# Kernel optimization log

Measured on AMD Instinct MI355X. Metric: run time of the kernel, lower is better.

Reference implementation:

```python
import jax, jax.numpy as jnp
import numpy as np

# ---- model constants (match init_kwargs) ----
E = 128; GH = 8; GD = E // GH; GL = 3          # graph emb / heads / layers
SH = 4; SD = E // SH; SL = 4                   # sequence transformer
ATOM = 64; BOND = 16; RBF_K = 32; CUTOFF = 5.0
VOCAB = 64; SEQL = 128
N = 32                                          # nodes per graph (equal-size graphs)
GC = 64; GS = 16; BMOL = 16; DEG = 64; GF = 3   # conf graphs / scaffold graphs / molecules / edges-per-graph
LN_EPS = 1e-5
CENTERS = jnp.linspace(0.0, CUTOFF, RBF_K)
GAMMA = (CUTOFF / (RBF_K - 1)) ** -2            # GaussianRBF gamma = (center spacing)^-2


def _ln(x, g, b):
    mu = x.mean(-1, keepdims=True)
    var = ((x - mu) ** 2).mean(-1, keepdims=True)
    return (x - mu) / jnp.sqrt(var + LN_EPS) * g + b


def _graph_encoder(x, edge_index, edge_attr, pos, G, p):
    # node projection
    h = x @ p["gproj_w"] + p["gproj_b"]                      # [G*N, E]
    # edge features: bond features + RBF(distance)
    d = jnp.clip(edge_attr[:, -1], 0.0, 10.0)
    rbf = jnp.exp(-GAMMA * (d[:, None] - CENTERS) ** 2)       # [M, K]
    ef = jnp.concatenate([edge_attr[:, :-1], rbf], axis=1)    # [M, BOND+K]
    # EdgeNetwork: per-edge matrix (gather -> matvec -> scatter-add)
    M = ef.shape[0]
    m = (ef @ p["elin_w"] + p["elin_b"]).reshape(M, E, E)
    msg = jnp.einsum("mef,mf->me", m, h[edge_index[1]])      # [M, E]
    aggr = jnp.zeros_like(h).at[edge_index[0]].add(msg)
    h = _ln(h + aggr, p["eln_g"], p["eln_b"])
    # dense per-graph layout (equal-size graphs -> reshape, mask is all-true)
    hb = h.reshape(G, N, E)
    pp = pos.reshape(G, N, 3)
    d2 = jnp.sum((pp[:, :, None, :] - pp[:, None, :, :]) ** 2, axis=-1)
    dist = jnp.where(d2 > 0, jnp.sqrt(jnp.where(d2 > 0, d2, 1.0)), 0.0)  # safe cdist
    inv_sqrt_d = 1.0 / np.sqrt(GD)
    for l in range(GL):
        def heads(t):
            return t.reshape(G, N, GH, GD).transpose(0, 2, 1, 3)
        q = heads(hb @ p["gt_qw"][l] + p["gt_qb"][l])
        k = heads(hb @ p["gt_kw"][l] + p["gt_kb"][l])
        v = heads(hb @ p["gt_vw"][l] + p["gt_vb"][l])
        s = jnp.einsum("bhnd,bhmd->bhnm", q, k) * inv_sqrt_d + dist[:, None]
        s = jnp.clip(s, -10.0, 10.0)
        a = jax.nn.softmax(s, axis=-1)                       # all nodes valid -> no mask
        o = jnp.einsum("bhnm,bhmd->bhnd", a, v).transpose(0, 2, 1, 3).reshape(G, N, E)
        o = o @ p["gt_ow"][l] + p["gt_ob"][l]
        x1 = _ln(hb + o, p["gt_ln1g"][l], p["gt_ln1b"][l])
        ff = jax.nn.relu(x1 @ p["gt_f1w"][l] + p["gt_f1b"][l]) @ p["gt_f2w"][l] + p["gt_f2b"][l]
        hb = _ln(x1 + ff, p["gt_ln2g"][l], p["gt_ln2b"][l])
    # masked mean pool with the source's eps in the denominator
    return hb.sum(1) / (N + 1e-8)


def _seq_encoder(tokens, p):
    B, L = tokens.shape
    x = p["tok_emb"][tokens] + p["pos_emb"][:L][None]        # [B, L, E]
    inv_sqrt_d = 1.0 / np.sqrt(SD)
    for l in range(SL):
        qkv = x @ p["se_inw"][l] + p["se_inb"][l]            # [B, L, 3E]
        q, k, v = jnp.split(qkv, 3, axis=-1)
        def heads(t):
            return t.reshape(B, L, SH, SD).transpose(0, 2, 1, 3)
        q, k, v = heads(q), heads(k), heads(v)
        a = jax.nn.softmax(jnp.einsum("bhnd,bhmd->bhnm", q, k) * inv_sqrt_d, axis=-1)
        o = jnp.einsum("bhnm,bhmd->bhnd", a, v).transpose(0, 2, 1, 3).reshape(B, L, E)
        o = o @ p["se_ow"][l] + p["se_ob"][l]
        x = _ln(x + o, p["se_ln1g"][l], p["se_ln1b"][l])      # post-norm (torch default)
        ff = jax.nn.relu(x @ p["se_f1w"][l] + p["se_f1b"][l]) @ p["se_f2w"][l] + p["se_f2b"][l]
        x = _ln(x + ff, p["se_ln2g"][l], p["se_ln2b"][l])
    return x.mean(1)                                          # [B, E]


def _forward(p, conf_edge_index, scaf_edge_index, tokens, conf_per_mol):
    g_all = _graph_encoder(p["conf_x"], conf_edge_index, p["conf_edge_attr"], p["conf_pos"], GC, p)
    conf_emb = g_all.reshape(-1, conf_per_mol, E).mean(1)     # per-molecule conformer mean (equal counts)
    scaf_emb = _graph_encoder(p["scaf_x"], scaf_edge_index, p["scaf_edge_attr"], p["scaf_pos"], GS, p)
    total = conf_emb + scaf_emb
    seq = _seq_encoder(tokens, p)
    # FusionGating
    gate_h = jax.nn.relu(jnp.concatenate([total, seq], -1) @ p["fg1_w"] + p["fg1_b"])
    gate = jax.nn.sigmoid(gate_h @ p["fg2_w"] + p["fg2_b"])
    fused = gate * total + (1.0 - gate) * seq
    # CrossModalAttention: MHA over a length-1 sequence (unsqueeze(0)) -> softmax
    # weights are identically 1, so attn(q_in, kv, kv) == out_proj(v_proj(kv)).
    g, s = fused, fused
    for l in range(2):
        g2s = (s @ p["cm_g2s_vw"][l] + p["cm_g2s_vb"][l]) @ p["cm_g2s_ow"][l] + p["cm_g2s_ob"][l]
        g = _ln(g + g2s, p["cm_n1g"][l], p["cm_n1b"][l])
        s2g = (g @ p["cm_s2g_vw"][l] + p["cm_s2g_vb"][l]) @ p["cm_s2g_ow"][l] + p["cm_s2g_ob"][l]
        s = _ln(s + s2g, p["cm_n2g"][l], p["cm_n2b"][l])
    final = (g + s) * 0.5
    comb = jnp.concatenate([final, p["graph_features"]], -1)
    return (jax.nn.relu(comb @ p["r1_w"] + p["r1_b"]) @ p["r2_w"] + p["r2_b"])[:, 0]


def setup_inputs() -> dict:
    ks = iter(jax.random.split(jax.random.key(0), 64))
    def nrm(shape, s):
        return (jax.random.normal(next(ks), shape) * s).astype(jnp.float32)
    inp = {}
    def mk_graph(prefix, G):
        inp[prefix + "_x"] = nrm((G * N, ATOM), 1.0)
        off = (jnp.arange(G) * N)[:, None]
        src = jax.random.randint(next(ks), (G, DEG), 0, N) + off   # within-graph edges
        dst = jax.random.randint(next(ks), (G, DEG), 0, N) + off
        inp[prefix + "_edge_index"] = jnp.stack([src.ravel(), dst.ravel()]).astype(jnp.int32)
        bond = jax.random.uniform(next(ks), (G * DEG, BOND))
        dist = jax.random.uniform(next(ks), (G * DEG, 1), minval=0.5, maxval=CUTOFF)
        inp[prefix + "_edge_attr"] = jnp.concatenate([bond, dist], 1).astype(jnp.float32)
        inp[prefix + "_pos"] = nrm((G * N, 3), 2.0)
    mk_graph("conf", GC)
    mk_graph("scaf", GS)
    inp["tokens"] = jax.random.randint(next(ks), (BMOL, SEQL), 1, VOCAB).astype(jnp.int32)
    inp["graph_features"] = nrm((BMOL, GF), 1.0)
    inp["conf_per_mol"] = GC // BMOL
    W = 0.05
    inp["gproj_w"] = nrm((ATOM, E), W); inp["gproj_b"] = jnp.zeros(E)
    inp["elin_w"] = nrm((BOND + RBF_K, E * E), W); inp["elin_b"] = jnp.zeros(E * E)
    inp["eln_g"] = jnp.ones(E); inp["eln_b"] = jnp.zeros(E)
    for nm in ["qw", "kw", "vw", "ow"]:
        inp["gt_" + nm] = nrm((GL, E, E), W)
        inp["gt_" + nm[0] + "b"] = jnp.zeros((GL, E))
    inp["gt_ln1g"] = jnp.ones((GL, E)); inp["gt_ln1b"] = jnp.zeros((GL, E))
    inp["gt_f1w"] = nrm((GL, E, 2 * E), W); inp["gt_f1b"] = jnp.zeros((GL, 2 * E))
    inp["gt_f2w"] = nrm((GL, 2 * E, E), W); inp["gt_f2b"] = jnp.zeros((GL, E))
    inp["gt_ln2g"] = jnp.ones((GL, E)); inp["gt_ln2b"] = jnp.zeros((GL, E))
    inp["tok_emb"] = nrm((VOCAB, E), 0.02); inp["pos_emb"] = nrm((256, E), 0.02)
    inp["se_inw"] = nrm((SL, E, 3 * E), W); inp["se_inb"] = jnp.zeros((SL, 3 * E))
    inp["se_ow"] = nrm((SL, E, E), W); inp["se_ob"] = jnp.zeros((SL, E))
    inp["se_ln1g"] = jnp.ones((SL, E)); inp["se_ln1b"] = jnp.zeros((SL, E))
    inp["se_f1w"] = nrm((SL, E, 2 * E), W); inp["se_f1b"] = jnp.zeros((SL, 2 * E))
    inp["se_f2w"] = nrm((SL, 2 * E, E), W); inp["se_f2b"] = jnp.zeros((SL, E))
    inp["se_ln2g"] = jnp.ones((SL, E)); inp["se_ln2b"] = jnp.zeros((SL, E))
    inp["fg1_w"] = nrm((2 * E, 64), W); inp["fg1_b"] = jnp.zeros(64)
    inp["fg2_w"] = nrm((64, E), W); inp["fg2_b"] = jnp.zeros(E)
    for nm in ["g2s", "s2g"]:
        inp["cm_" + nm + "_vw"] = nrm((2, E, E), W); inp["cm_" + nm + "_vb"] = jnp.zeros((2, E))
        inp["cm_" + nm + "_ow"] = nrm((2, E, E), W); inp["cm_" + nm + "_ob"] = jnp.zeros((2, E))
    inp["cm_n1g"] = jnp.ones((2, E)); inp["cm_n1b"] = jnp.zeros((2, E))
    inp["cm_n2g"] = jnp.ones((2, E)); inp["cm_n2b"] = jnp.zeros((2, E))
    inp["r1_w"] = nrm((E + GF, E), W); inp["r1_b"] = jnp.zeros(E)
    inp["r2_w"] = nrm((E, 1), W); inp["r2_b"] = jnp.zeros(1)
    return inp


def reference(conf_x, conf_edge_attr, conf_pos, scaf_x, scaf_edge_attr, scaf_pos, graph_features,
              gproj_w, gproj_b, elin_w, elin_b, eln_g, eln_b,
              gt_qw, gt_qb, gt_kw, gt_kb, gt_vw, gt_vb, gt_ow, gt_ob,
              gt_ln1g, gt_ln1b, gt_f1w, gt_f1b, gt_f2w, gt_f2b, gt_ln2g, gt_ln2b,
              tok_emb, pos_emb,
              se_inw, se_inb, se_ow, se_ob, se_ln1g, se_ln1b, se_f1w, se_f1b, se_f2w, se_f2b, se_ln2g, se_ln2b,
              fg1_w, fg1_b, fg2_w, fg2_b,
              cm_g2s_vw, cm_g2s_vb, cm_g2s_ow, cm_g2s_ob, cm_n1g, cm_n1b,
              cm_s2g_vw, cm_s2g_vb, cm_s2g_ow, cm_s2g_ob, cm_n2g, cm_n2b,
              r1_w, r1_b, r2_w, r2_b,
              conf_edge_index, scaf_edge_index, tokens, conf_per_mol):
    p = dict(locals())
    return _forward(p, conf_edge_index, scaf_edge_index, tokens, conf_per_mol)
```

## Files before the change

### kernel.cpp

```cpp
#include <hip/hip_runtime.h>
#include <hip/hip_bf16.h>


struct __align__(16) G16Sm   { float Sa[32][20]; float Bs[32][136]; };
struct __align__(16) GAttnSm { float qs[32][17], ksh[32][17], vsh[32][17], ss[32][33], rs[32]; };
struct __align__(16) SAttnSm { float kv[32][33], qs2[32][33], ss2[32][129], red[32][8], red2[32][8]; };
struct __align__(16) TailSm  { float x1[16][132]; float hid[16][260]; float sbuf[4352]; float Sa[32][20]; };
union AttnU { GAttnSm a; SAttnSm s; };

__device__ __forceinline__ float blk_norm(float v, int e, float* sred)
{
  float s = v;
  #pragma unroll
  for (int o = 1; o < 64; o <<= 1) s += __shfl_xor(s, o);
  if ((e & 63) == 0) sred[e >> 6] = s;
  __syncthreads();
  float mean = (sred[0] + sred[1]) * (1.0f / 128.0f);
  __syncthreads();
  float d = v - mean;
  float s2 = d * d;
  #pragma unroll
  for (int o = 1; o < 64; o <<= 1) s2 += __shfl_xor(s2, o);
  if ((e & 63) == 0) sred[e >> 6] = s2;
  __syncthreads();
  float var = (sred[0] + sred[1]) * (1.0f / 128.0f);
  __syncthreads();
  return d / sqrtf(var + 1e-5f);
}

__global__ __launch_bounds__(256) void front_k(
    const float* __restrict__ cx, const float* __restrict__ sx,
    const float* __restrict__ w, const float* __restrict__ b,
    float* __restrict__ h, float* __restrict__ aggr,
    const float* __restrict__ cpos, const float* __restrict__ spos, float* __restrict__ dist,
    const int* __restrict__ tokens, const float* __restrict__ tok_emb,
    const float* __restrict__ pos_emb, float* __restrict__ xs)
{
  __shared__ float sP[128];
  const int bx = blockIdx.x, tid = threadIdx.x;
  if (bx < 1280) {
    int r = bx * 2 + (tid >> 7), e = tid & 127;
    const float* x = (r < 2048) ? (cx + (size_t)r * 64) : (sx + (size_t)(r - 2048) * 64);
    float* xrow = sP + (tid >> 7) * 64;
    if (e < 64) xrow[e] = x[e];
    __syncthreads();
    float acc = b[e];
    for (int a = 0; a < 64; a++) acc += xrow[a] * w[a * 128 + e];
    h[(size_t)r * 128 + e] = acc;
    aggr[(size_t)r * 128 + e] = 0.0f;
  } else if (bx < 1360) {
    int g = bx - 1280;
    const float* p = (g < 64) ? (cpos + (size_t)g * 96) : (spos + (size_t)(g - 64) * 96);
    if (tid < 96) sP[tid] = p[tid];
    __syncthreads();
    #pragma unroll
    for (int jj = 0; jj < 4; jj++) {
      int idx = tid * 4 + jj;
      int i = idx >> 5, j = idx & 31;
      float dx = sP[i * 3 + 0] - sP[j * 3 + 0];
      float dy = sP[i * 3 + 1] - sP[j * 3 + 1];
      float dz = sP[i * 3 + 2] - sP[j * 3 + 2];
      float d2 = dx * dx + dy * dy + dz * dz;
      dist[(size_t)g * 1024 + idx] = (d2 > 0.0f) ? sqrtf(d2) : 0.0f;
    }
  } else {
    int r = (bx - 1360) * 2 + (tid >> 7), e = tid & 127;
    int tk = tokens[r];
    xs[(size_t)r * 128 + e] = tok_emb[(size_t)tk * 128 + e] + pos_emb[(size_t)(r & 127) * 128 + e];
  }
}

__global__ __launch_bounds__(256) void edge_gemm_k(
    const float* __restrict__ cea, const float* __restrict__ sea,
    const int* __restrict__ cei, const int* __restrict__ sei,
    const float* __restrict__ h,
    const float* __restrict__ elw, const float* __restrict__ elb,
    float* __restrict__ aggr)
{
  __shared__ float efs[32][8];
  __shared__ float As[32][36];
  __shared__ float Bs[32][136];
  const int tid = threadIdx.x;
  const int m0 = blockIdx.x * 32;
  const int kt0 = blockIdx.y * 28;
  const int c0 = kt0 >> 2;
  {
    int t = tid >> 3, cc = tid & 7;
    if (cc < 7) {
      int c = c0 + cc;
      int m = m0 + t;
      const float* attr = (m < 4096) ? (cea + (size_t)m * 17) : (sea + (size_t)(m - 4096) * 17);
      float val;
      if (c < 16) val = attr[c];
      else if (c < 48) {
        float d = fminf(fmaxf(attr[16], 0.0f), 10.0f);
        float t2 = d - (float)((c - 16) * (5.0 / 31.0));
        val = expf(-38.44f * t2 * t2);
      } else val = 1.0f;
      efs[t][cc] = val;
    }
  }
  const int gk = tid & 31, gt = (tid >> 5) * 4;
  float hreg[4][4];
  #pragma unroll
  for (int i = 0; i < 4; i++) {
    int m = m0 + gt + i;
    int dst = (m < 4096) ? cei[4096 + m] : (sei[1024 + (m - 4096)] + 2048);
    const float* hp = h + (size_t)dst * 128 + gk;
    hreg[i][0] = hp[0]; hreg[i][1] = hp[32]; hreg[i][2] = hp[64]; hreg[i][3] = hp[96];
  }
  const int tn = tid & 31, tm = tid >> 5;
  const int e0 = 4 * tn, t0 = 4 * tm;
  const int se = tid >> 1, sk = (tid & 1) * 16;
  float acc[4][4] = {};
  __syncthreads();
  #pragma unroll 1
  for (int kt = kt0; kt < kt0 + 28; kt++) {
    int c = kt >> 2, cc = c - c0, j = kt & 3;
    float4 av;
    av.x = efs[gt + 0][cc] * hreg[0][j];
    av.y = efs[gt + 1][cc] * hreg[1][j];
    av.z = efs[gt + 2][cc] * hreg[2][j];
    av.w = efs[gt + 3][cc] * hreg[3][j];
    *(float4*)&As[gk][gt] = av;
    const float* bp = ((c < 48) ? (elw + (size_t)c * 16384) : elb) + (size_t)se * 128 + j * 32 + sk;
    float4 w0 = *(const float4*)(bp + 0);
    float4 w1 = *(const float4*)(bp + 4);
    float4 w2 = *(const float4*)(bp + 8);
    float4 w3 = *(const float4*)(bp + 12);
    Bs[sk + 0][se] = w0.x;  Bs[sk + 1][se] = w0.y;  Bs[sk + 2][se] = w0.z;  Bs[sk + 3][se] = w0.w;
    Bs[sk + 4][se] = w1.x;  Bs[sk + 5][se] = w1.y;  Bs[sk + 6][se] = w1.z;  Bs[sk + 7][se] = w1.w;
    Bs[sk + 8][se] = w2.x;  Bs[sk + 9][se] = w2.y;  Bs[sk + 10][se] = w2.z; Bs[sk + 11][se] = w2.w;
    Bs[sk + 12][se] = w3.x; Bs[sk + 13][se] = w3.y; Bs[sk + 14][se] = w3.z; Bs[sk + 15][se] = w3.w;
    __syncthreads();
    #pragma unroll
    for (int kk = 0; kk < 32; kk++) {
      float4 a = *(const float4*)&As[kk][t0];
      float4 b = *(const float4*)&Bs[kk][e0];
      acc[0][0] += a.x * b.x; acc[0][1] += a.x * b.y; acc[0][2] += a.x * b.z; acc[0][3] += a.x * b.w;
      acc[1][0] += a.y * b.x; acc[1][1] += a.y * b.y; acc[1][2] += a.y * b.z; acc[1][3] += a.y * b.w;
      acc[2][0] += a.z * b.x; acc[2][1] += a.z * b.y; acc[2][2] += a.z * b.z; acc[2][3] += a.z * b.w;
      acc[3][0] += a.w * b.x; acc[3][1] += a.w * b.y; acc[3][2] += a.w * b.z; acc[3][3] += a.w * b.w;
    }
    __syncthreads();
  }
  #pragma unroll
  for (int i = 0; i < 4; i++) {
    int m = m0 + t0 + i;
    int src = (m < 4096) ? cei[m] : (sei[m - 4096] + 2048);
    float* dst = aggr + (size_t)src * 128 + e0;
    atomicAdd(dst + 0, acc[i][0]);
    atomicAdd(dst + 1, acc[i][1]);
    atomicAdd(dst + 2, acc[i][2]);
    atomicAdd(dst + 3, acc[i][3]);
  }
}

__device__ __forceinline__ void gemm16_body(G16Sm& sm,
    const float* __restrict__ A, const float* __restrict__ Bp,
    const float* __restrict__ biasp, float* __restrict__ Cp,
    int row0, int ldb, int ldc)
{
  const int tid = threadIdx.x;
  const int tm = tid >> 5, tn = tid & 31;
  const int t0 = 2 * tm, e0 = 4 * tn;
  const int ar = tid >> 4, ak = (tid & 15) * 2;
  const int bk = tid >> 3, be = (tid & 7) * 16;
  float acc[2][4] = {};
  for (int k0 = 0; k0 < 128; k0 += 32) {
    float2 av = *(const float2*)(A + (size_t)(row0 + ar) * 128 + k0 + ak);
    sm.Sa[ak][ar] = av.x; sm.Sa[ak + 1][ar] = av.y;
    const float* bp = Bp + (size_t)(k0 + bk) * ldb + be;
    float4 b0v = *(const float4*)(bp + 0);
    float4 b1v = *(const float4*)(bp + 4);
    float4 b2v = *(const float4*)(bp + 8);
    float4 b3v = *(const float4*)(bp + 12);
    sm.Bs[bk][be + 0] = b0v.x;  sm.Bs[bk][be + 1] = b0v.y;  sm.Bs[bk][be + 2] = b0v.z;  sm.Bs[bk][be + 3] = b0v.w;
    sm.Bs[bk][be + 4] = b1v.x;  sm.Bs[bk][be + 5] = b1v.y;  sm.Bs[bk][be + 6] = b1v.z;  sm.Bs[bk][be + 7] = b1v.w;
    sm.Bs[bk][be + 8] = b2v.x;  sm.Bs[bk][be + 9] = b2v.y;  sm.Bs[bk][be + 10] = b2v.z; sm.Bs[bk][be + 11] = b2v.w;
    sm.Bs[bk][be + 12] = b3v.x; sm.Bs[bk][be + 13] = b3v.y; sm.Bs[bk][be + 14] = b3v.z; sm.Bs[bk][be + 15] = b3v.w;
    __syncthreads();
    #pragma unroll
    for (int kk = 0; kk < 32; kk++) {
      float2 a = *(const float2*)&sm.Sa[kk][t0];
      float4 b = *(const float4*)&sm.Bs[kk][e0];
      acc[0][0] += a.x * b.x; acc[0][1] += a.x * b.y; acc[0][2] += a.x * b.z; acc[0][3] += a.x * b.w;
      acc[1][0] += a.y * b.x; acc[1][1] += a.y * b.y; acc[1][2] += a.y * b.z; acc[1][3] += a.y * b.w;
    }
    __syncthreads();
  }
  #pragma unroll
  for (int i = 0; i < 2; i++) {
    float* cp = Cp + (size_t)(row0 + t0 + i) * ldc + e0;
    #pragma unroll
    for (int j = 0; j < 4; j++) cp[j] = acc[i][j] + biasp[e0 + j];
  }
}

__global__ __launch_bounds__(256) void qkv_k(
    int gBlocks,
    const float* __restrict__ ghb,
    const float* gqw, const float* gkw, const float* gvw,
    const float* gqb, const float* gkb, const float* gvb, float* gout,
    const float* __restrict__ sxs, const float* sw, const float* sb, float* sout)
{
  __shared__ G16Sm sm;
  int bx = blockIdx.x;
  if (bx < gBlocks) {
    int z = bx / 160, rt = bx % 160;
    const float* B = (z == 0) ? gqw : (z == 1) ? gkw : gvw;
    const float* bias = (z == 0) ? gqb : (z == 1) ? gkb : gvb;
    gemm16_body(sm, ghb, B, bias, gout + (size_t)z * 327680, rt * 16, 128, 128);
  } else {
    int i = bx - gBlocks;
    int z = i >> 7, rt = i & 127;
    gemm16_body(sm, sxs, sw + z * 128, sb + z * 128, sout + z * 128, rt * 16, 384, 384);
  }
}

__device__ __forceinline__ void gattn_body(GAttnSm& sm, int g, int h,
    const float* __restrict__ q, const float* __restrict__ k,
    const float* __restrict__ v, const float* __restrict__ dist, float* __restrict__ o)
{
  const int tid = threadIdx.x;
  {
    int idx = tid * 2;
    int i = idx >> 4, d = idx & 15;
    size_t base = ((size_t)(g * 32 + i)) * 128 + h * 16 + d;
    sm.qs[i][d] = q[base];  sm.qs[i][d + 1] = q[base + 1];
    sm.ksh[i][d] = k[base]; sm.ksh[i][d + 1] = k[base + 1];
    sm.vsh[i][d] = v[base]; sm.vsh[i][d + 1] = v[base + 1];
  }
  __syncthreads();
  {
    int i = tid >> 3, j0 = (tid & 7) * 4;
    for (int j = j0; j < j0 + 4; j++) {
      float a = 0;
      #pragma unroll
      for (int d = 0; d < 16; d++) a += sm.qs[i][d] * sm.ksh[j][d];
      a = a * 0.25f + dist[(size_t)g * 1024 + i * 32 + j];
      sm.ss[i][j] = fminf(fmaxf(a, -10.0f), 10.0f);
    }
  }
  __syncthreads();
  if (tid < 32) {
    float m = -1e30f;
    for (int j = 0; j < 32; j++) m = fmaxf(m, sm.ss[tid][j]);
    float s = 0;
    for (int j = 0; j < 32; j++) { float ex = expf(sm.ss[tid][j] - m); sm.ss[tid][j] = ex; s += ex; }
    sm.rs[tid] = 1.0f / s;
  }
  __syncthreads();
  {
    int idx = tid * 2;
    int i = idx >> 4, d = idx & 15;
    float a0 = 0, a1 = 0;
    for (int j = 0; j < 32; j++) { float wj = sm.ss[i][j]; a0 += wj * sm.vsh[j][d]; a1 += wj * sm.vsh[j][d + 1]; }
    float r = sm.rs[i];
    size_t base = ((size_t)(g * 32 + i)) * 128 + h * 16 + d;
    o[base] = a0 * r; o[base + 1] = a1 * r;
  }
}

__device__ __forceinline__ void sattn_body(SAttnSm& sm, int b, int h, int qt,
    const float* __restrict__ qkv, float* __restrict__ o)
{
  const int tid = threadIdx.x;
  {
    int i = tid >> 3, d0 = (tid & 7) * 4;
    const float* qp = qkv + ((size_t)(b * 128 + qt * 32 + i)) * 384 + h * 32 + d0;
    sm.qs2[i][d0 + 0] = qp[0]; sm.qs2[i][d0 + 1] = qp[1];
    sm.qs2[i][d0 + 2] = qp[2]; sm.qs2[i][d0 + 3] = qp[3];
  }
  const int i = tid >> 3, sub = tid & 7;
  for (int jt = 0; jt < 4; jt++) {
    {
      int r = tid >> 3, dd = (tid & 7) * 4;
      const float* kp = qkv + ((size_t)(b * 128 + jt * 32 + r)) * 384 + 128 + h * 32 + dd;
      float4 kv4 = *(const float4*)kp;
      sm.kv[r][dd + 0] = kv4.x; sm.kv[r][dd + 1] = kv4.y;
      sm.kv[r][dd + 2] = kv4.z; sm.kv[r][dd + 3] = kv4.w;
    }
    __syncthreads();
    {
      int j0 = jt * 32 + sub * 4;
      for (int j = j0; j < j0 + 4; j++) {
        int jr = j - jt * 32;
        float a = 0;
        #pragma unroll
        for (int d = 0; d < 32; d++) a += sm.qs2[i][d] * sm.kv[jr][d];
        sm.ss2[i][j] = a * 0.17677669529663687f;
      }
    }
    __syncthreads();
  }
  float m = -1e30f;
  for (int j = sub; j < 128; j += 8) m = fmaxf(m, sm.ss2[i][j]);
  sm.red[i][sub] = m;
  __syncthreads();
  float mm = sm.red[i][0];
  #pragma unroll
  for (int t = 1; t < 8; t++) mm = fmaxf(mm, sm.red[i][t]);
  float ps = 0;
  for (int j = sub; j < 128; j += 8) { float ex = expf(sm.ss2[i][j] - mm); sm.ss2[i][j] = ex; ps += ex; }
  sm.red2[i][sub] = ps;
  __syncthreads();
  float s = 0;
  #pragma unroll
  for (int t = 0; t < 8; t++) s += sm.red2[i][t];
  float rinv = 1.0f / s;
  float a0 = 0, a1 = 0, a2 = 0, a3 = 0;
  const int d0 = sub * 4;
  for (int jt = 0; jt < 4; jt++) {
    __syncthreads();
    {
      int r = tid >> 3, dd = (tid & 7) * 4;
      const float* vp = qkv + ((size_t)(b * 128 + jt * 32 + r)) * 384 + 256 + h * 32 + dd;
      float4 vv = *(const float4*)vp;
      sm.kv[r][dd + 0] = vv.x; sm.kv[r][dd + 1] = vv.y;
      sm.kv[r][dd + 2] = vv.z; sm.kv[r][dd + 3] = vv.w;
    }
    __syncthreads();
    for (int jr = 0; jr < 32; jr++) {
      float wj = sm.ss2[i][jt * 32 + jr];
      a0 += wj * sm.kv[jr][d0 + 0]; a1 += wj * sm.kv[jr][d0 + 1];
      a2 += wj * sm.kv[jr][d0 + 2]; a3 += wj * sm.kv[jr][d0 + 3];
    }
  }
  float* op = o + ((size_t)(b * 128 + qt * 32 + i)) * 128 + h * 32 + d0;
  op[0] = a0 * rinv; op[1] = a1 * rinv; op[2] = a2 * rinv; op[3] = a3 * rinv;
}

__global__ __launch_bounds__(256) void attn_k(
    int gBlocks, const float* q, const float* k, const float* v,
    const float* dist, float* go, const float* qkv, float* so)
{
  __shared__ AttnU u;
  int bx = blockIdx.x;
  if (bx < gBlocks) gattn_body(u.a, bx >> 3, bx & 7, q, k, v, dist, go);
  else { int i = bx - gBlocks; sattn_body(u.s, i >> 4, (i >> 2) & 3, i & 3, qkv, so); }
}

__device__ __forceinline__ void tail_body(TailSm& sm, int row0, const float* __restrict__ A,
    const float* __restrict__ Wo, const float* __restrict__ bo, const float* __restrict__ res,
    const float* __restrict__ g1, const float* __restrict__ b1n,
    const float* __restrict__ W1, const float* __restrict__ b1f,
    const float* __restrict__ W2, const float* __restrict__ b2f,
    const float* __restrict__ g2, const float* __restrict__ b2n,
    float* __restrict__ Out)
{
  float (*BsA)[136] = (float(*)[136])sm.sbuf;
  float (*Bs1)[260] = (float(*)[260])sm.sbuf;
  float (*Bs2)[136] = (float(*)[136])sm.sbuf;
  const int tid = threadIdx.x;
  {
    const int tm = tid >> 5, tn = tid & 31;
    const int t0 = 2 * tm, e0 = 4 * tn;
    const int ar = tid >> 4, ak = (tid & 15) * 2;
    const int bk = tid >> 3, be = (tid & 7) * 16;
    float acc[2][4] = {};
    for (int k0 = 0; k0 < 128; k0 += 32) {
      float2 av = *(const float2*)(A + (size_t)(row0 + ar) * 128 + k0 + ak);
      sm.Sa[ak][ar] = av.x; sm.Sa[ak + 1][ar] = av.y;
      const float* bp = Wo + (size_t)(k0 + bk) * 128 + be;
      float4 b0v = *(const float4*)(bp + 0);
      float4 b1v = *(const float4*)(bp + 4);
      float4 b2v = *(const float4*)(bp + 8);
      float4 b3v = *(const float4*)(bp + 12);
      BsA[bk][be + 0] = b0v.x;  BsA[bk][be + 1] = b0v.y;  BsA[bk][be + 2] = b0v.z;  BsA[bk][be + 3] = b0v.w;
      BsA[bk][be + 4] = b1v.x;  BsA[bk][be + 5] = b1v.y;  BsA[bk][be + 6] = b1v.z;  BsA[bk][be + 7] = b1v.w;
      BsA[bk][be + 8] = b2v.x;  BsA[bk][be + 9] = b2v.y;  BsA[bk][be + 10] = b2v.z; BsA[bk][be + 11] = b2v.w;
      BsA[bk][be + 12] = b3v.x; BsA[bk][be + 13] = b3v.y; BsA[bk][be + 14] = b3v.z; BsA[bk][be + 15] = b3v.w;
      __syncthreads();
      #pragma unroll
      for (int kk = 0; kk < 32; kk++) {
        float2 a = *(const float2*)&sm.Sa[kk][t0];
        float4 b = *(const float4*)&BsA[kk][e0];
        acc[0][0] += a.x * b.x; acc[0][1] += a.x * b.y; acc[0][2] += a.x * b.z; acc[0][3] += a.x * b.w;
        acc[1][0] += a.y * b.x; acc[1][1] += a.y * b.y; acc[1][2] += a.y * b.z; acc[1][3] += a.y * b.w;
      }
      __syncthreads();
    }
    #pragma unroll
    for (int i = 0; i < 2; i++) {
      int r = row0 + t0 + i;
      float v0 = acc[i][0] + bo[e0 + 0] + res[(size_t)r * 128 + e0 + 0];
      float v1 = acc[i][1] + bo[e0 + 1] + res[(size_t)r * 128 + e0 + 1];
      float v2 = acc[i][2] + bo[e0 + 2] + res[(size_t)r * 128 + e0 + 2];
      float v3 = acc[i][3] + bo[e0 + 3] + res[(size_t)r * 128 + e0 + 3];
      float s = v0 + v1 + v2 + v3;
      #pragma unroll
      for (int o = 1; o < 32; o <<= 1) s += __shfl_xor(s, o);
      float mean = s * (1.0f / 128.0f);
      float d0 = v0 - mean, d1 = v1 - mean, d2 = v2 - mean, d3 = v3 - mean;
      float sq = d0 * d0 + d1 * d1 + d2 * d2 + d3 * d3;
      #pragma unroll
      for (int o = 1; o < 32; o <<= 1) sq += __shfl_xor(sq, o);
      float rstd = 1.0f / sqrtf(sq * (1.0f / 128.0f) + 1e-5f);
      sm.x1[t0 + i][e0 + 0] = d0 * rstd * g1[e0 + 0] + b1n[e0 + 0];
      sm.x1[t0 + i][e0 + 1] = d1 * rstd * g1[e0 + 1] + b1n[e0 + 1];
      sm.x1[t0 + i][e0 + 2] = d2 * rstd * g1[e0 + 2] + b1n[e0 + 2];
      sm.x1[t0 + i][e0 + 3] = d3 * rstd * g1[e0 + 3] + b1n[e0 + 3];
    }
  }
  __syncthreads();
  {
    const int tm = tid >> 6, tn = tid & 63;
    const int t0 = 4 * tm, e0 = 4 * tn;
    const int ar = tid >> 4, ak = tid & 15;
    const int bk = tid >> 4, be = (tid & 15) * 16;
    float acc[4][4] = {};
    for (int k0 = 0; k0 < 128; k0 += 16) {
      sm.Sa[ak][ar] = sm.x1[ar][k0 + ak];
      const float* bp = W1 + (size_t)(k0 + bk) * 256 + be;
      float4 b0v = *(const float4*)(bp + 0);
      float4 b1v = *(const float4*)(bp + 4);
      float4 b2v = *(const float4*)(bp + 8);
      float4 b3v = *(const float4*)(bp + 12);
      Bs1[bk][be + 0] = b0v.x;  Bs1[bk][be + 1] = b0v.y;  Bs1[bk][be + 2] = b0v.z;  Bs1[bk][be + 3] = b0v.w;
      Bs1[bk][be + 4] = b1v.x;  Bs1[bk][be + 5] = b1v.y;  Bs1[bk][be + 6] = b1v.z;  Bs1[bk][be + 7] = b1v.w;
      Bs1[bk][be + 8] = b2v.x;  Bs1[bk][be + 9] = b2v.y;  Bs1[bk][be + 10] = b2v.z; Bs1[bk][be + 11] = b2v.w;
      Bs1[bk][be + 12] = b3v.x; Bs1[bk][be + 13] = b3v.y; Bs1[bk][be + 14] = b3v.z; Bs1[bk][be + 15] = b3v.w;
      __syncthreads();
      #pragma unroll
      for (int kk = 0; kk < 16; kk++) {
        float4 a = *(const float4*)&sm.Sa[kk][t0];
        float4 b = *(const float4*)&Bs1[kk][e0];
        acc[0][0] += a.x * b.x; acc[0][1] += a.x * b.y; acc[0][2] += a.x * b.z; acc[0][3] += a.x * b.w;
        acc[1][0] += a.y * b.x; acc[1][1] += a.y * b.y; acc[1][2] += a.y * b.z; acc[1][3] += a.y * b.w;
        acc[2][0] += a.z * b.x; acc[2][1] += a.z * b.y; acc[2][2] += a.z * b.z; acc[2][3] += a.z * b.w;
        acc[3][0] += a.w * b.x; acc[3][1] += a.w * b.y; acc[3][2] += a.w * b.z; acc[3][3] += a.w * b.w;
      }
      __syncthreads();
    }
    #pragma unroll
    for (int i = 0; i < 4; i++) {
      float4 hv;
      hv.x = fmaxf(acc[i][0] + b1f[e0 + 0], 0.0f);
      hv.y = fmaxf(acc[i][1] + b1f[e0 + 1], 0.0f);
      hv.z = fmaxf(acc[i][2] + b1f[e0 + 2], 0.0f);
      hv.w = fmaxf(acc[i][3] + b1f[e0 + 3], 0.0f);
      *(float4*)&sm.hid[t0 + i][e0] = hv;
    }
  }
  __syncthreads();
  {
    const int tm = tid >> 5, tn = tid & 31;
    const int t0 = 2 * tm, e0 = 4 * tn;
    const int bk = tid >> 3, be = (tid & 7) * 16;
    float acc[2][4] = {};
    for (int k0 = 0; k0 < 256; k0 += 32) {
      const float* bp = W2 + (size_t)(k0 + bk) * 128 + be;
      float4 b0v = *(const float4*)(bp + 0);
      float4 b1v = *(const float4*)(bp + 4);
      float4 b2v = *(const float4*)(bp + 8);
      float4 b3v = *(const float4*)(bp + 12);
      Bs2[bk][be + 0] = b0v.x;  Bs2[bk][be + 1] = b0v.y;  Bs2[bk][be + 2] = b0v.z;  Bs2[bk][be + 3] = b0v.w;
      Bs2[bk][be + 4] = b1v.x;  Bs2[bk][be + 5] = b1v.y;  Bs2[bk][be + 6] = b1v.z;  Bs2[bk][be + 7] = b1v.w;
      Bs2[bk][be + 8] = b2v.x;  Bs2[bk][be + 9] = b2v.y;  Bs2[bk][be + 10] = b2v.z; Bs2[bk][be + 11] = b2v.w;
      Bs2[bk][be + 12] = b3v.x; Bs2[bk][be + 13] = b3v.y; Bs2[bk][be + 14] = b3v.z; Bs2[bk][be + 15] = b3v.w;
      __syncthreads();
      #pragma unroll
      for (int kk = 0; kk < 32; kk++) {
        float a0 = sm.hid[t0 + 0][k0 + kk];
        float a1 = sm.hid[t0 + 1][k0 + kk];
        float4 b = *(const float4*)&Bs2[kk][e0];
        acc[0][0] += a0 * b.x; acc[0][1] += a0 * b.y; acc[0][2] += a0 * b.z; acc[0][3] += a0 * b.w;
        acc[1][0] += a1 * b.x; acc[1][1] += a1 * b.y; acc[1][2] += a1 * b.z; acc[1][3] += a1 * b.w;
      }
      __syncthreads();
    }
    #pragma unroll
    for (int i = 0; i < 2; i++) {
      int r = row0 + t0 + i;
      float v0 = acc[i][0] + b2f[e0 + 0] + sm.x1[t0 + i][e0 + 0];
      float v1 = acc[i][1] + b2f[e0 + 1] + sm.x1[t0 + i][e0 + 1];
      float v2 = acc[i][2] + b2f[e0 + 2] + sm.x1[t0 + i][e0 + 2];
      float v3 = acc[i][3] + b2f[e0 + 3] + sm.x1[t0 + i][e0 + 3];
      float s = v0 + v1 + v2 + v3;
      #pragma unroll
      for (int o = 1; o < 32; o <<= 1) s += __shfl_xor(s, o);
      float mean = s * (1.0f / 128.0f);
      float d0 = v0 - mean, d1 = v1 - mean, d2 = v2 - mean, d3 = v3 - mean;
      float sq = d0 * d0 + d1 * d1 + d2 * d2 + d3 * d3;
      #pragma unroll
      for (int o = 1; o < 32; o <<= 1) sq += __shfl_xor(sq, o);
      float rstd = 1.0f / sqrtf(sq * (1.0f / 128.0f) + 1e-5f);
      float* cp = Out + (size_t)r * 128 + e0;
      cp[0] = d0 * rstd * g2[e0 + 0] + b2n[e0 + 0];
      cp[1] = d1 * rstd * g2[e0 + 1] + b2n[e0 + 1];
      cp[2] = d2 * rstd * g2[e0 + 2] + b2n[e0 + 2];
      cp[3] = d3 * rstd * g2[e0 + 3] + b2n[e0 + 3];
    }
  }
}

__global__ __launch_bounds__(256) void tail_k(
    int gBlocks,
    const float* gA, const float* gWo, const float* gbo, const float* gres,
    const float* gg1, const float* gb1, const float* gW1, const float* gbf1,
    const float* gW2, const float* gbf2, const float* gg2, const float* gb2, float* gOut,
    const float* sA, const float* sWo, const float* sbo, const float* sres,
    const float* sg1, const float* sb1, const float* sW1, const float* sbf1,
    const float* sW2, const float* sbf2, const float* sg2, const float* sb2, float* sOut)
{
  __shared__ TailSm sm;
  int bx = blockIdx.x;
  if (bx < gBlocks)
    tail_body(sm, bx * 16, gA, gWo, gbo, gres, gg1, gb1, gW1, gbf1, gW2, gbf2, gg2, gb2, gOut);
  else
    tail_body(sm, (bx - gBlocks) * 16, sA, sWo, sbo, sres, sg1, sb1, sW1, sbf1, sW2, sbf2, sg2, sb2, sOut);
}

__global__ __launch_bounds__(128) void ln_k(
    const float* __restrict__ x, const float* __restrict__ res,
    const float* __restrict__ g, const float* __restrict__ b, float* __restrict__ out)
{
  __shared__ float sred[2];
  int r = blockIdx.x, e = threadIdx.x;
  size_t idx = (size_t)r * 128 + e;
  float v = x[idx] + res[idx];
  float nv = blk_norm(v, e, sred);
  out[idx] = nv * g[e] + b[e];
}

__global__ __launch_bounds__(128) void head_k(
    const float* __restrict__ hb, const float* __restrict__ xs, const float* __restrict__ gfeat,
    const float* fg1w, const float* fg1b, const float* fg2w, const float* fg2b,
    const float* g2s_vw, const float* g2s_vb, const float* g2s_ow, const float* g2s_ob,
    const float* n1g, const float* n1b,
    const float* s2g_vw, const float* s2g_vb, const float* s2g_ow, const float* s2g_ob,
    const float* n2g, const float* n2b,
    const float* r1w, const float* r1b, const float* r2w, const float* r2b,
    float* __restrict__ out)
{
  __shared__ float T[128], S[128], G[128], Sm[128], t1[128], t2[128], gh[64], sred[2];
  int mol = blockIdx.x, e = threadIdx.x;
  {
    float cs = 0;
    for (int c = 0; c < 4; c++) {
      int g = mol * 4 + c;
      float s = 0;
      for (int i = 0; i < 32; i++) s += hb[((size_t)(g * 32 + i)) * 128 + e];
      cs += s * (1.0f / 32.0f);
    }
    cs *= 0.25f;
    float s2 = 0;
    int g = 64 + mol;
    for (int i = 0; i < 32; i++) s2 += hb[((size_t)(g * 32 + i)) * 128 + e];
    T[e] = cs + s2 * (1.0f / 32.0f);
    float ss = 0;
    for (int l = 0; l < 128; l++) ss += xs[((size_t)(mol * 128 + l)) * 128 + e];
    S[e] = ss * (1.0f / 128.0f);
  }
  __syncthreads();
  if (e < 64) {
    float a = fg1b[e];
    for (int f = 0; f < 128; f++) a += T[f] * fg1w[f * 64 + e];
    for (int f = 0; f < 128; f++) a += S[f] * fg1w[(128 + f) * 64 + e];
    gh[e] = fmaxf(a, 0.0f);
  }
  __syncthreads();
  {
    float a = fg2b[e];
    for (int j = 0; j < 64; j++) a += gh[j] * fg2w[j * 128 + e];
    float gate = 1.0f / (1.0f + expf(-a));
    float fu = gate * T[e] + (1.0f - gate) * S[e];
    G[e] = fu; Sm[e] = fu;
  }
  __syncthreads();
  for (int l = 0; l < 2; l++) {
    const float* vw = g2s_vw + (size_t)l * 16384; const float* vb = g2s_vb + l * 128;
    const float* ow = g2s_ow + (size_t)l * 16384; const float* ob = g2s_ob + l * 128;
    float a = vb[e];
    for (int f = 0; f < 128; f++) a += Sm[f] * vw[f * 128 + e];
    t1[e] = a;
    __syncthreads();
    a = ob[e];
    for (int f = 0; f < 128; f++) a += t1[f] * ow[f * 128 + e];
    float nv = blk_norm(G[e] + a, e, sred);
    G[e] = nv * n1g[l * 128 + e] + n1b[l * 128 + e];
    __syncthreads();
    const float* vw2 = s2g_vw + (size_t)l * 16384; const float* vb2 = s2g_vb + l * 128;
    const float* ow2 = s2g_ow + (size_t)l * 16384; const float* ob2 = s2g_ob + l * 128;
    a = vb2[e];
    for (int f = 0; f < 128; f++) a += G[f] * vw2[f * 128 + e];
    t1[e] = a;
    __syncthreads();
    a = ob2[e];
    for (int f = 0; f < 128; f++) a += t1[f] * ow2[f * 128 + e];
    nv = blk_norm(Sm[e] + a, e, sred);
    Sm[e] = nv * n2g[l * 128 + e] + n2b[l * 128 + e];
    __syncthreads();
  }
  t2[e] = 0.5f * (G[e] + Sm[e]);
  __syncthreads();
  float a = r1b[e];
  for (int f = 0; f < 128; f++) a += t2[f] * r1w[f * 128 + e];
  for (int f = 0; f < 3; f++) a += gfeat[mol * 3 + f] * r1w[(128 + f) * 128 + e];
  a = fmaxf(a, 0.0f);
  float p = a * r2w[e];
  #pragma unroll
  for (int o = 1; o < 64; o <<= 1) p += __shfl_xor(p, o);
  if ((e & 63) == 0) sred[e >> 6] = p;
  __syncthreads();
  if (e == 0) out[mol] = sred[0] + sred[1] + r2b[0];
}

extern "C" void kernel_launch(void* const* d_in, const int* in_sizes, int n_in,
                              void* d_out, int out_size, void* d_ws, size_t ws_size,
                              hipStream_t stream)
{
  (void)n_in; (void)out_size; (void)ws_size;
  const bool dict = (in_sizes[1] == 8192);
  auto IN = [&](int di, int si) { return d_in[dict ? di : si]; };

  const float* conf_x   = (const float*)IN(0, 0);
  const int*   conf_ei  = (const int*)  IN(1, 63);
  const float* conf_ea  = (const float*)IN(2, 1);
  const float* conf_pos = (const float*)IN(3, 2);
  const float* scaf_x   = (const float*)IN(4, 3);
  const int*   scaf_ei  = (const int*)  IN(5, 64);
  const float* scaf_ea  = (const float*)IN(6, 4);
  const float* scaf_pos = (const float*)IN(7, 5);
  const int*   tokens   = (const int*)  IN(8, 65);
  const float* gfeat    = (const float*)IN(9, 6);
  const float* gproj_w  = (const float*)IN(11, 7);
  const float* gproj_b  = (const float*)IN(12, 8);
  const float* elin_w   = (const float*)IN(13, 9);
  const float* elin_b   = (const float*)IN(14, 10);
  const float* eln_g    = (const float*)IN(15, 11);
  const float* eln_b    = (const float*)IN(16, 12);
  const float* gt_qw    = (const float*)IN(17, 13);
  const float* gt_qb    = (const float*)IN(18, 14);
  const float* gt_kw    = (const float*)IN(19, 15);
  const float* gt_kb    = (const float*)IN(20, 16);
  const float* gt_vw    = (const float*)IN(21, 17);
  const float* gt_vb    = (const float*)IN(22, 18);
  const float* gt_ow    = (const float*)IN(23, 19);
  const float* gt_ob    = (const float*)IN(24, 20);
  const float* gt_ln1g  = (const float*)IN(25, 21);
  const float* gt_ln1b  = (const float*)IN(26, 22);
  const float* gt_f1w   = (const float*)IN(27, 23);
  const float* gt_f1b   = (const float*)IN(28, 24);
  const float* gt_f2w   = (const float*)IN(29, 25);
  const float* gt_f2b   = (const float*)IN(30, 26);
  const float* gt_ln2g  = (const float*)IN(31, 27);
  const float* gt_ln2b  = (const float*)IN(32, 28);
  const float* tok_emb  = (const float*)IN(33, 29);
  const float* pos_emb  = (const float*)IN(34, 30);
  const float* se_inw   = (const float*)IN(35, 31);
  const float* se_inb   = (const float*)IN(36, 32);
  const float* se_ow    = (const float*)IN(37, 33);
  const float* se_ob    = (const float*)IN(38, 34);
  const float* se_ln1g  = (const float*)IN(39, 35);
  const float* se_ln1b  = (const float*)IN(40, 36);
  const float* se_f1w   = (const float*)IN(41, 37);
  const float* se_f1b   = (const float*)IN(42, 38);
  const float* se_f2w   = (const float*)IN(43, 39);
  const float* se_f2b   = (const float*)IN(44, 40);
  const float* se_ln2g  = (const float*)IN(45, 41);
  const float* se_ln2b  = (const float*)IN(46, 42);
  const float* fg1_w    = (const float*)IN(47, 43);
  const float* fg1_b    = (const float*)IN(48, 44);
  const float* fg2_w    = (const float*)IN(49, 45);
  const float* fg2_b    = (const float*)IN(50, 46);
  const float* cm_g2s_vw = (const float*)IN(51, 47);
  const float* cm_g2s_vb = (const float*)IN(52, 48);
  const float* cm_g2s_ow = (const float*)IN(53, 49);
  const float* cm_g2s_ob = (const float*)IN(54, 50);
  const float* cm_s2g_vw = (const float*)IN(55, 53);
  const float* cm_s2g_vb = (const float*)IN(56, 54);
  const float* cm_s2g_ow = (const float*)IN(57, 55);
  const float* cm_s2g_ob = (const float*)IN(58, 56);
  const float* cm_n1g   = (const float*)IN(59, 51);
  const float* cm_n1b   = (const float*)IN(60, 52);
  const float* cm_n2g   = (const float*)IN(61, 57);
  const float* cm_n2b   = (const float*)IN(62, 58);
  const float* r1_w     = (const float*)IN(63, 59);
  const float* r1_b     = (const float*)IN(64, 60);
  const float* r2_w     = (const float*)IN(65, 61);
  const float* r2_b     = (const float*)IN(66, 62);
  float* out = (float*)d_out;

  float* w = (float*)d_ws;
  size_t off = 0;
  auto alloc = [&](size_t n) { float* p = w + off; off += n; return p; };
  float* h     = alloc(2560 * 128);
  float* aggr  = alloc(2560 * 128);
  float* hb    = alloc(2560 * 128);
  float* distb = alloc(80 * 1024);
  float* qb    = alloc(3 * 327680);
  float* atto  = alloc(327680);
  float* xs2   = alloc(2048 * 128);
  float* qkv3  = alloc(2048 * 384);
  float* satto = alloc(2048 * 128);
  float* xsfin = alloc(2048 * 128);

  front_k<<<2384, 256, 0, stream>>>(conf_x, scaf_x, gproj_w, gproj_b, h, aggr,
                                    conf_pos, scaf_pos, distb,
                                    tokens, tok_emb, pos_emb, xs2);
  edge_gemm_k<<<dim3(160, 7), 256, 0, stream>>>(conf_ea, scaf_ea, conf_ei, scaf_ei, h, elin_w, elin_b, aggr);
  ln_k<<<2560, 128, 0, stream>>>(aggr, h, eln_g, eln_b, hb);

  for (int l = 0; l < 4; l++) {
    const bool hasG = (l < 3);
    const int lg = hasG ? l : 0;
    const int gq = hasG ? 480 : 0;
    const int ga = hasG ? 640 : 0;
    const int gt = hasG ? 160 : 0;
    float* sOut = (l == 3) ? xsfin : xs2;
    qkv_k<<<gq + 384, 256, 0, stream>>>(gq,
        hb, gt_qw + (size_t)lg * 16384, gt_kw + (size_t)lg * 16384, gt_vw + (size_t)lg * 16384,
        gt_qb + lg * 128, gt_kb + lg * 128, gt_vb + lg * 128, qb,
        xs2, se_inw + (size_t)l * 49152, se_inb + l * 384, qkv3);
    attn_k<<<ga + 256, 256, 0, stream>>>(ga, qb, qb + 327680, qb + 655360, distb, atto, qkv3, satto);
    tail_k<<<gt + 128, 256, 0, stream>>>(gt,
        atto, gt_ow + (size_t)lg * 16384, gt_ob + lg * 128, hb,
        gt_ln1g + lg * 128, gt_ln1b + lg * 128,
        gt_f1w + (size_t)lg * 32768, gt_f1b + lg * 256,
        gt_f2w + (size_t)lg * 32768, gt_f2b + lg * 128,
        gt_ln2g + lg * 128, gt_ln2b + lg * 128, hb,
        satto, se_ow + (size_t)l * 16384, se_ob + l * 128, xs2,
        se_ln1g + l * 128, se_ln1b + l * 128,
        se_f1w + (size_t)l * 32768, se_f1b + l * 256,
        se_f2w + (size_t)l * 32768, se_f2b + l * 128,
        se_ln2g + l * 128, se_ln2b + l * 128, sOut);
  }

  head_k<<<16, 128, 0, stream>>>(hb, xsfin, gfeat,
                                 fg1_w, fg1_b, fg2_w, fg2_b,
                                 cm_g2s_vw, cm_g2s_vb, cm_g2s_ow, cm_g2s_ob, cm_n1g, cm_n1b,
                                 cm_s2g_vw, cm_s2g_vb, cm_s2g_ow, cm_s2g_ob, cm_n2g, cm_n2b,
                                 r1_w, r1_b, r2_w, r2_b, out);
}
```

Baseline: 628.6 us.

## Factorize edge network into per-node GEMM plus per-edge weighted combine

Replaces the per-edge matrix GEMM with a factorized form: first compute, for every node, h multiplied by each of the 48 edge-weight slices plus the bias (a 2560x6272 intermediate), then for each edge combine those 49 vectors with the edge features and scatter-add into the aggregate. This cuts the FLOPs, since nodes (2560) are fewer than edges (5120) and the big weight tensor is applied once per node, not once per edge. It needs a large workspace buffer, which is checked against ws_size with the old path kept as fallback. It also adds an extra pass writing and reading a roughly 64MB intermediate.

```diff
diff --git a/kernel.cpp b/kernel.cpp
--- a/kernel.cpp
+++ b/kernel.cpp
@@ -153,6 +153,103 @@
     atomicAdd(dst + 1, acc[i][1]);
     atomicAdd(dst + 2, acc[i][2]);
     atomicAdd(dst + 3, acc[i][3]);
+  }
+}
+
+__global__ __launch_bounds__(256) void node_gemm_k(
+    const float* __restrict__ h, const float* __restrict__ elw, const float* __restrict__ elb,
+    float* __restrict__ G)
+{
+  __shared__ float As[32][36];
+  __shared__ float Bs[32][136];
+  const int tid = threadIdx.x;
+  const int n0 = blockIdx.x * 32;
+  const int c = blockIdx.y;
+  const float* W = (c < 48) ? (elw + (size_t)c * 16384) : elb;
+  const int gk = tid & 31, gt = (tid >> 5) * 4;
+  float hreg[4][4];
+  #pragma unroll
+  for (int i = 0; i < 4; i++) {
+    const float* hp = h + (size_t)(n0 + gt + i) * 128 + gk;
+    hreg[i][0] = hp[0]; hreg[i][1] = hp[32]; hreg[i][2] = hp[64]; hreg[i][3] = hp[96];
+  }
+  const int tn = tid & 31, tm = tid >> 5;
+  const int e0 = 4 * tn, t0 = 4 * tm;
+  const int se = tid >> 1, sk = (tid & 1) * 16;
+  float acc[4][4] = {};
+  #pragma unroll 1
+  for (int j = 0; j < 4; j++) {
+    float4 av;
+    av.x = hreg[0][j]; av.y = hreg[1][j]; av.z = hreg[2][j]; av.w = hreg[3][j];
+    *(float4*)&As[gk][gt] = av;
+    const float* bp = W + (size_t)se * 128 + j * 32 + sk;
+    float4 w0 = *(const float4*)(bp + 0);
+    float4 w1 = *(const float4*)(bp + 4);
+    float4 w2 = *(const float4*)(bp + 8);
+    float4 w3 = *(const float4*)(bp + 12);
+    Bs[sk + 0][se] = w0.x;  Bs[sk + 1][se] = w0.y;  Bs[sk + 2][se] = w0.z;  Bs[sk + 3][se] = w0.w;
+    Bs[sk + 4][se] = w1.x;  Bs[sk + 5][se] = w1.y;  Bs[sk + 6][se] = w1.z;  Bs[sk + 7][se] = w1.w;
+    Bs[sk + 8][se] = w2.x;  Bs[sk + 9][se] = w2.y;  Bs[sk + 10][se] = w2.z; Bs[sk + 11][se] = w2.w;
+    Bs[sk + 12][se] = w3.x; Bs[sk + 13][se] = w3.y; Bs[sk + 14][se] = w3.z; Bs[sk + 15][se] = w3.w;
+    __syncthreads();
+    #pragma unroll
+    for (int kk = 0; kk < 32; kk++) {
+      float4 a = *(const float4*)&As[kk][t0];
+      float4 b = *(const float4*)&Bs[kk][e0];
+      acc[0][0] += a.x * b.x; acc[0][1] += a.x * b.y; acc[0][2] += a.x * b.z; acc[0][3] += a.x * b.w;
+      acc[1][0] += a.y * b.x; acc[1][1] += a.y * b.y; acc[1][2] += a.y * b.z; acc[1][3] += a.y * b.w;
+      acc[2][0] += a.z * b.x; acc[2][1] += a.z * b.y; acc[2][2] += a.z * b.z; acc[2][3] += a.z * b.w;
+      acc[3][0] += a.w * b.x; acc[3][1] += a.w * b.y; acc[3][2] += a.w * b.z; acc[3][3] += a.w * b.w;
+    }
+    __syncthreads();
+  }
+  #pragma unroll
+  for (int i = 0; i < 4; i++) {
+    float4 cv;
+    cv.x = acc[i][0]; cv.y = acc[i][1]; cv.z = acc[i][2]; cv.w = acc[i][3];
+    *(float4*)(G + (size_t)(n0 + t0 + i) * 6272 + c * 128 + e0) = cv;
+  }
+}
+
+__global__ __launch_bounds__(256) void combine_k(
+    const float* __restrict__ cea, const float* __restrict__ sea,
+    const int* __restrict__ cei, const int* __restrict__ sei,
+    const float* __restrict__ G, float* __restrict__ aggr)
+{
+  __shared__ float efs[4][52];
+  __shared__ int srcs[4], dsts[4];
+  const int tid = threadIdx.x;
+  const int m0 = blockIdx.x * 4;
+  if (tid < 4) {
+    int m = m0 + tid;
+    int src, dst;
+    if (m < 4096) { src = cei[m]; dst = cei[4096 + m]; }
+    else { src = sei[m - 4096] + 2048; dst = sei[1024 + (m - 4096)] + 2048; }
+    srcs[tid] = src; dsts[tid] = dst;
+  }
+  if (tid < 196) {
+    int t = tid / 49, cc = tid - t * 49;
+    int m = m0 + t;
+    const float* attr = (m < 4096) ? (cea + (size_t)m * 17) : (sea + (size_t)(m - 4096) * 17);
+    float val;
+    if (cc < 16) val = attr[cc];
+    else if (cc < 48) {
+      float d = fminf(fmaxf(attr[16], 0.0f), 10.0f);
+      float t2 = d - (float)((cc - 16) * (5.0 / 31.0));
+      val = expf(-38.44f * t2 * t2);
+    } else val = 1.0f;
+    efs[t][cc] = val;
+  }
+  __syncthreads();
+  const int e = tid & 127, half = tid >> 7;
+  #pragma unroll
+  for (int tt = 0; tt < 2; tt++) {
+    int t = half * 2 + tt;
+    const float* gp = G + (size_t)dsts[t] * 6272 + e;
+    float acc = 0;
+    #pragma unroll 7
+    for (int c = 0; c < 49; c++) acc += efs[t][c] * gp[(size_t)c * 128];
+    atomicAdd(aggr + (size_t)srcs[t] * 128 + e, acc);
   }
 }
 
@@ -611,7 +708,7 @@
                               void* d_out, int out_size, void* d_ws, size_t ws_size,
                               hipStream_t stream)
 {
-  (void)n_in; (void)out_size; (void)ws_size;
+  (void)n_in; (void)out_size;
   const bool dict = (in_sizes[1] == 8192);
   auto IN = [&](int di, int si) { return d_in[dict ? di : si]; };
 
@@ -696,11 +793,19 @@
   float* qkv3  = alloc(2048 * 384);
   float* satto = alloc(2048 * 128);
   float* xsfin = alloc(2048 * 128);
+  float* Gws   = w + off;
+  const size_t needed = (off + (size_t)2560 * 6272) * sizeof(float);
+  const bool factorized = (ws_size >= needed);
 
   front_k<<<2384, 256, 0, stream>>>(conf_x, scaf_x, gproj_w, gproj_b, h, aggr,
                                     conf_pos, scaf_pos, distb,
                                     tokens, tok_emb, pos_emb, xs2);
-  edge_gemm_k<<<dim3(160, 7), 256, 0, stream>>>(conf_ea, scaf_ea, conf_ei, scaf_ei, h, elin_w, elin_b, aggr);
+  if (factorized) {
+    node_gemm_k<<<dim3(80, 49), 256, 0, stream>>>(h, elin_w, elin_b, Gws);
+    combine_k<<<1280, 256, 0, stream>>>(conf_ea, scaf_ea, conf_ei, scaf_ei, Gws, aggr);
+  } else {
+    edge_gemm_k<<<dim3(160, 7), 256, 0, stream>>>(conf_ea, scaf_ea, conf_ei, scaf_ei, h, elin_w, elin_b, aggr);
+  }
   ln_k<<<2560, 128, 0, stream>>>(aggr, h, eln_g, eln_b, hb);
 
   for (int l = 0; l < 4; l++) {
```

After: 554.4 us. 1.13x faster.
